# Kernel tuning notes

Hardware: AMD Instinct MI355X
Metric: run time of the kernel (lower is better)

The kernel has to match this reference:

```python
import jax, jax.numpy as jnp
import numpy as np

N_HEADS = 16


def setup_inputs() -> dict:
    key = jax.random.key(0)
    ks = jax.random.split(key, 7)
    B, S, D = 2, 2048, 1024
    x = jax.random.normal(ks[0], (B, S, D), dtype=jnp.float32)
    attn_mask = jax.random.normal(ks[1], (S, S), dtype=jnp.float32) * 0.1
    attn_bias = jax.random.normal(ks[2], (B, S, S), dtype=jnp.float32) * 0.1
    Wqkv = jax.random.normal(ks[3], (D, 3 * D), dtype=jnp.float32) * (D ** -0.5)
    bqkv = jnp.zeros((3 * D,), dtype=jnp.float32)
    Wout = jax.random.normal(ks[4], (D, D), dtype=jnp.float32) * (D ** -0.5)
    bout = jnp.zeros((D,), dtype=jnp.float32)
    return {"x": x, "attn_mask": attn_mask, "attn_bias": attn_bias,
            "Wqkv": Wqkv, "bqkv": bqkv, "Wout": Wout, "bout": bout}


def reference(x, attn_mask, attn_bias, Wqkv, bqkv, Wout, bout):
    B, S, D = x.shape
    H = N_HEADS
    hd = D // H
    # qkv projection: [B,S,3D] -> [3,B,H,S,hd]
    qkv = (x @ Wqkv + bqkv).reshape(B, S, 3, H, hd).transpose(2, 0, 3, 1, 4)
    q, k, v = qkv[0], qkv[1], qkv[2]
    scores = jnp.einsum('bhqd,bhkd->bhqk', q, k) / (hd ** 0.5)
    scores = scores + attn_mask[None, None, :, :] + attn_bias[:, None, :, :]
    attn = jax.nn.softmax(scores, axis=-1)  # dropout p=0.0 (eval)
    out = jnp.einsum('bhqk,bhkd->bhqd', attn, v)
    out = out.transpose(0, 2, 1, 3).reshape(B, S, D)
    return out @ Wout + bout
```

## Files before the change

kernel.cpp:

```cpp
#include <hip/hip_runtime.h>
#include <hip/hip_bf16.h>


#define S_LEN 2048
#define DMODEL 1024
#define NH 16
#define HD 64

typedef __bf16 bf16x8 __attribute__((ext_vector_type(8)));
typedef __bf16 bf16x4 __attribute__((ext_vector_type(4)));
typedef __bf16 bf16x2v __attribute__((ext_vector_type(2)));
typedef float f32x4 __attribute__((ext_vector_type(4)));

#define GLD_LDS16(g, l)                                              \
  __builtin_amdgcn_global_load_lds(                                  \
      (const __attribute__((address_space(1))) unsigned int*)(g),    \
      (__attribute__((address_space(3))) unsigned int*)(l), 16, 0, 0)

__global__ __launch_bounds__(256) void cvt_x(const float* __restrict__ X,
                                             __bf16* __restrict__ Xb) {
  int i = blockIdx.x * 256 + threadIdx.x;
  float4 v = ((const float4*)X)[i];
  bf16x4 o = {(__bf16)v.x, (__bf16)v.y, (__bf16)v.z, (__bf16)v.w};
  *(bf16x4*)&Xb[(size_t)i * 4] = o;
}

__global__ __launch_bounds__(256) void cvt_wt(const float* __restrict__ W,
                                              __bf16* __restrict__ Wt,
                                              int ncols) {
  __shared__ float tile[64][65];
  const int n0 = blockIdx.x * 64;
  const int k0 = blockIdx.y * 64;
  const int tid = threadIdx.x;
  {
    int c = tid & 63, r4 = tid >> 6;
#pragma unroll
    for (int p = 0; p < 16; ++p) {
      int r = r4 + p * 4;
      tile[r][c] = W[(size_t)(k0 + r) * ncols + n0 + c];
    }
  }
  __syncthreads();
  {
    int cc = (tid & 31) * 2, r8 = tid >> 5;
#pragma unroll
    for (int p = 0; p < 8; ++p) {
      int rr = r8 + p * 8;
      bf16x2v o = {(__bf16)tile[cc][rr], (__bf16)tile[cc + 1][rr]};
      *(bf16x2v*)&Wt[(size_t)(n0 + rr) * 1024 + k0 + cc] = o;
    }
  }
}

__global__ __launch_bounds__(256) void mb_fuse(const float* __restrict__ mask,
                                               const float* __restrict__ bias,
                                               __bf16* __restrict__ MB) {
  const int kt = blockIdx.x, qt = blockIdx.y, b = blockIdx.z;
  const int tid = threadIdx.x;
  const int r = tid >> 2;
  const int c0 = (tid & 3) * 16;
  const size_t qrow = (size_t)(qt * 64 + r);
  const float* mp = mask + qrow * S_LEN + kt * 64 + c0;
  const float* bp =
      bias + (size_t)b * S_LEN * S_LEN + qrow * S_LEN + kt * 64 + c0;
  __bf16* op = MB + (((size_t)(b * 32 + qt) * 32 + kt) * 4096) + r * 64 + c0;
#pragma unroll
  for (int e = 0; e < 4; ++e) {
    float4 m = *(const float4*)(mp + e * 4);
    float4 a = *(const float4*)(bp + e * 4);
    bf16x4 o = {(__bf16)(m.x + a.x), (__bf16)(m.y + a.y), (__bf16)(m.z + a.z),
                (__bf16)(m.w + a.w)};
    *(bf16x4*)(op + e * 4) = o;
  }
}

__global__ __launch_bounds__(256) void gemm_qkv_mfma(
    const __bf16* __restrict__ Xb, const __bf16* __restrict__ Wt,
    const float* __restrict__ bqkv, __bf16* __restrict__ Qb,
    __bf16* __restrict__ Kb, __bf16* __restrict__ Vtb) {
  __shared__ __align__(16) __bf16 As[128 * 32];
  __shared__ __align__(16) __bf16 Bs[128 * 32];
  const int tid = threadIdx.x;
  const int w = tid >> 6, lane = tid & 63;
  const int c = lane & 15, quad = lane >> 4;
  const int wm = w >> 1, wn = w & 1;
  const int rowBase = blockIdx.y * 128;
  const int colBase = blockIdx.x * 128;

  f32x4 acc[4][4] = {};

  const __bf16* gA0 =
      Xb + (size_t)(rowBase + w * 32 + (lane >> 2)) * 1024 + (lane & 3) * 8;
  const __bf16* gB0 =
      Wt + (size_t)(colBase + w * 32 + (lane >> 2)) * 1024 + (lane & 3) * 8;
  __bf16* lA0 = &As[(w * 32) * 32];
  __bf16* lB0 = &Bs[(w * 32) * 32];

  for (int k0 = 0; k0 < 1024; k0 += 32) {
    __syncthreads();
#pragma unroll
    for (int p = 0; p < 2; ++p) {
      GLD_LDS16(gA0 + (size_t)p * 16 * 1024 + k0, lA0 + p * 16 * 32);
      GLD_LDS16(gB0 + (size_t)p * 16 * 1024 + k0, lB0 + p * 16 * 32);
    }
    __syncthreads();

    bf16x8 af[4], bfr[4];
#pragma unroll
    for (int mt = 0; mt < 4; ++mt)
      af[mt] = *(const bf16x8*)&As[(wm * 64 + mt * 16 + c) * 32 + quad * 8];
#pragma unroll
    for (int nt = 0; nt < 4; ++nt)
      bfr[nt] = *(const bf16x8*)&Bs[(wn * 64 + nt * 16 + c) * 32 + quad * 8];
#pragma unroll
    for (int mt = 0; mt < 4; ++mt)
#pragma unroll
      for (int nt = 0; nt < 4; ++nt)
        acc[mt][nt] = __builtin_amdgcn_mfma_f32_16x16x32_bf16(
            af[mt], bfr[nt], acc[mt][nt], 0, 0, 0);
  }

#pragma unroll
  for (int mt = 0; mt < 4; ++mt) {
    int row0 = rowBase + wm * 64 + mt * 16 + quad * 4;
#pragma unroll
    for (int nt = 0; nt < 4; ++nt) {
      int col = colBase + wn * 64 + nt * 16 + c;
      float bias = bqkv[col];
      int three = col >> 10;
      int h = (col & 1023) >> 6;
      int d = col & 63;
#pragma unroll
      for (int r = 0; r < 4; ++r) {
        int rr = row0 + r;
        int bb = rr >> 11, s = rr & 2047;
        float val = acc[mt][nt][r] + bias;
        size_t ho = (size_t)(bb * NH + h);
        if (three == 0)
          Qb[(ho * S_LEN + s) * HD + d] = (__bf16)val;
        else if (three == 1)
          Kb[(ho * S_LEN + s) * HD + d] = (__bf16)val;
        else
          Vtb[(ho * HD + d) * S_LEN + s] = (__bf16)val;
      }
    }
  }
}

__global__ __launch_bounds__(256) void attn_mfma(
    const __bf16* __restrict__ Qb, const __bf16* __restrict__ Kb,
    const __bf16* __restrict__ Vtb, const __bf16* __restrict__ MB,
    __bf16* __restrict__ AOb) {
  const int qt = blockIdx.x, h = blockIdx.y, b = blockIdx.z;
  const int tid = threadIdx.x;
  const int w = tid >> 6;
  const int lane = tid & 63;
  const int c = lane & 15;
  const int quad = lane >> 4;

  __shared__ __align__(16) __bf16 Ks[64 * 72];
  __shared__ __align__(16) __bf16 Vs[64 * 72];
  __shared__ __align__(16) __bf16 Ps[64 * 72];
  __shared__ __align__(16) __bf16 MBs[64 * 64];

  const int qbase = qt * 64;
  const size_t headoff = (size_t)(b * NH + h) * S_LEN * HD;
  const __bf16* Qg = Qb + headoff + (size_t)qbase * HD;
  const __bf16* Kg = Kb + headoff;
  const __bf16* Vg = Vtb + headoff;
  const __bf16* MBg = MB + ((size_t)(b * 32 + qt) * 32) * 4096;

  bf16x8 qa0 = *(const bf16x8*)(Qg + (w * 16 + c) * HD + quad * 8);
  bf16x8 qa1 = *(const bf16x8*)(Qg + (w * 16 + c) * HD + quad * 8 + 32);

  f32x4 Oa[4] = {};
  float lsum[4] = {0.f, 0.f, 0.f, 0.f};

  for (int kt = 0; kt < 32; ++kt) {
    const int kbase = kt * 64;
    __syncthreads();
    {
      const __bf16* Kt = Kg + (size_t)kbase * HD;
      const __bf16* MBt = MBg + (size_t)kt * 4096;
#pragma unroll
      for (int p = 0; p < 2; ++p) {
        int ch = p * 256 + tid;
        int f = ch >> 3, c8 = (ch & 7) * 8;
        *(uint4*)&Ks[f * 72 + c8] = ((const uint4*)Kt)[ch];
        *(uint4*)&Vs[f * 72 + c8] =
            *(const uint4*)(Vg + (size_t)f * S_LEN + kbase + c8);
        GLD_LDS16(MBt + (size_t)ch * 8, &MBs[ch * 8]);
      }
    }
    __syncthreads();

    f32x4 sv[4];
#pragma unroll
    for (int ct = 0; ct < 4; ++ct) {
      f32x4 a = {};
      bf16x8 kf0 = *(const bf16x8*)&Ks[(ct * 16 + c) * 72 + quad * 8];
      bf16x8 kf1 = *(const bf16x8*)&Ks[(ct * 16 + c) * 72 + quad * 8 + 32];
      a = __builtin_amdgcn_mfma_f32_16x16x32_bf16(qa0, kf0, a, 0, 0, 0);
      a = __builtin_amdgcn_mfma_f32_16x16x32_bf16(qa1, kf1, a, 0, 0, 0);
      sv[ct] = a;
    }
#pragma unroll
    for (int ct = 0; ct < 4; ++ct)
#pragma unroll
      for (int r = 0; r < 4; ++r) {
        float mb = (float)MBs[(w * 16 + quad * 4 + r) * 64 + ct * 16 + c];
        float p = __expf(sv[ct][r] * 0.125f + mb - 8.0f);
        sv[ct][r] = p;
        lsum[r] += p;
        Ps[(w * 16 + quad * 4 + r) * 72 + ct * 16 + c] = (__bf16)p;
      }
    bf16x8 pf0 = *(const bf16x8*)&Ps[(w * 16 + c) * 72 + quad * 8];
    bf16x8 pf1 = *(const bf16x8*)&Ps[(w * 16 + c) * 72 + quad * 8 + 32];
#pragma unroll
    for (int ft = 0; ft < 4; ++ft) {
      bf16x8 vf0 = *(const bf16x8*)&Vs[(ft * 16 + c) * 72 + quad * 8];
      bf16x8 vf1 = *(const bf16x8*)&Vs[(ft * 16 + c) * 72 + quad * 8 + 32];
      Oa[ft] =
          __builtin_amdgcn_mfma_f32_16x16x32_bf16(pf0, vf0, Oa[ft], 0, 0, 0);
      Oa[ft] =
          __builtin_amdgcn_mfma_f32_16x16x32_bf16(pf1, vf1, Oa[ft], 0, 0, 0);
    }
  }
  float invl[4];
#pragma unroll
  for (int r = 0; r < 4; ++r) {
    float t = lsum[r];
    t += __shfl_xor(t, 1);
    t += __shfl_xor(t, 2);
    t += __shfl_xor(t, 4);
    t += __shfl_xor(t, 8);
    invl[r] = 1.0f / t;
  }
#pragma unroll
  for (int ft = 0; ft < 4; ++ft)
#pragma unroll
    for (int r = 0; r < 4; ++r)
      AOb[(size_t)(b * S_LEN + qbase + w * 16 + quad * 4 + r) * DMODEL +
          h * HD + ft * 16 + c] = (__bf16)(Oa[ft][r] * invl[r]);
}

__global__ __launch_bounds__(256) void gemm_out_mfma(
    const __bf16* __restrict__ AOb, const __bf16* __restrict__ Wt2,
    const float* __restrict__ bout, float* __restrict__ Out) {
  __shared__ __align__(16) __bf16 As[128 * 32];
  __shared__ __align__(16) __bf16 Bs[128 * 32];
  const int tid = threadIdx.x;
  const int w = tid >> 6, lane = tid & 63;
  const int c = lane & 15, quad = lane >> 4;
  const int wm = w >> 1, wn = w & 1;
  const int rowBase = blockIdx.y * 128;
  const int colBase = blockIdx.x * 128;

  f32x4 acc[4][4] = {};

  const __bf16* gA0 =
      AOb + (size_t)(rowBase + w * 32 + (lane >> 2)) * 1024 + (lane & 3) * 8;
  const __bf16* gB0 =
      Wt2 + (size_t)(colBase + w * 32 + (lane >> 2)) * 1024 + (lane & 3) * 8;
  __bf16* lA0 = &As[(w * 32) * 32];
  __bf16* lB0 = &Bs[(w * 32) * 32];

  for (int k0 = 0; k0 < 1024; k0 += 32) {
    __syncthreads();
#pragma unroll
    for (int p = 0; p < 2; ++p) {
      GLD_LDS16(gA0 + (size_t)p * 16 * 1024 + k0, lA0 + p * 16 * 32);
      GLD_LDS16(gB0 + (size_t)p * 16 * 1024 + k0, lB0 + p * 16 * 32);
    }
    __syncthreads();

    bf16x8 af[4], bfr[4];
#pragma unroll
    for (int mt = 0; mt < 4; ++mt)
      af[mt] = *(const bf16x8*)&As[(wm * 64 + mt * 16 + c) * 32 + quad * 8];
#pragma unroll
    for (int nt = 0; nt < 4; ++nt)
      bfr[nt] = *(const bf16x8*)&Bs[(wn * 64 + nt * 16 + c) * 32 + quad * 8];
#pragma unroll
    for (int mt = 0; mt < 4; ++mt)
#pragma unroll
      for (int nt = 0; nt < 4; ++nt)
        acc[mt][nt] = __builtin_amdgcn_mfma_f32_16x16x32_bf16(
            af[mt], bfr[nt], acc[mt][nt], 0, 0, 0);
  }

#pragma unroll
  for (int mt = 0; mt < 4; ++mt) {
    int row0 = rowBase + wm * 64 + mt * 16 + quad * 4;
#pragma unroll
    for (int nt = 0; nt < 4; ++nt) {
      int col = colBase + wn * 64 + nt * 16 + c;
      float bias = bout[col];
#pragma unroll
      for (int r = 0; r < 4; ++r)
        Out[(size_t)(row0 + r) * 1024 + col] = acc[mt][nt][r] + bias;
    }
  }
}

extern "C" void kernel_launch(void* const* d_in, const int* in_sizes, int n_in,
                              void* d_out, int out_size, void* d_ws,
                              size_t ws_size, hipStream_t stream) {
  const float* x = (const float*)d_in[0];
  const float* attn_mask = (const float*)d_in[1];
  const float* attn_bias = (const float*)d_in[2];
  const float* Wqkv = (const float*)d_in[3];
  const float* bqkv = (const float*)d_in[4];
  const float* Wout = (const float*)d_in[5];
  const float* bout = (const float*)d_in[6];
  float* out = (float*)d_out;

  __bf16* base = (__bf16*)d_ws;
  __bf16* Xb = base;
  __bf16* AOb = base;
  __bf16* Wt = base + 4194304;
  __bf16* Qb = base + 8388608;
  __bf16* Kb = base + 12582912;
  __bf16* Vtb = base + 16777216;
  __bf16* MB = base + 20971520;
  __bf16* Wt2 = base + 29360128;

  cvt_x<<<4096, 256, 0, stream>>>(x, Xb);
  cvt_wt<<<dim3(48, 16), 256, 0, stream>>>(Wqkv, Wt, 3072);
  cvt_wt<<<dim3(16, 16), 256, 0, stream>>>(Wout, Wt2, 1024);
  mb_fuse<<<dim3(32, 32, 2), 256, 0, stream>>>(attn_mask, attn_bias, MB);
  gemm_qkv_mfma<<<dim3(24, 32), 256, 0, stream>>>(Xb, Wt, bqkv, Qb, Kb, Vtb);
  attn_mfma<<<dim3(32, NH, 2), 256, 0, stream>>>(Qb, Kb, Vtb, MB, AOb);
  gemm_out_mfma<<<dim3(8, 32), 256, 0, stream>>>(AOb, Wt2, bout, out);
}
```

Baseline: 312.9 us.

## Prefetch next K/V/mask tile into registers while computing current tile

```diff
diff --git a/kernel.cpp b/kernel.cpp
--- a/kernel.cpp
+++ b/kernel.cpp
@@ -161,7 +161,7 @@
   __shared__ __align__(16) __bf16 Ks[64 * 72];
   __shared__ __align__(16) __bf16 Vs[64 * 72];
   __shared__ __align__(16) __bf16 Ps[64 * 72];
-  __shared__ __align__(16) __bf16 MBs[64 * 64];
+  __shared__ __align__(16) __bf16 MBs[64 * 72];
 
   const int qbase = qt * 64;
   const size_t headoff = (size_t)(b * NH + h) * S_LEN * HD;
@@ -173,26 +173,43 @@
   bf16x8 qa0 = *(const bf16x8*)(Qg + (w * 16 + c) * HD + quad * 8);
   bf16x8 qa1 = *(const bf16x8*)(Qg + (w * 16 + c) * HD + quad * 8 + 32);
 
+  int f0 = tid >> 3, c80 = (tid & 7) * 8;
+  int f1 = (256 + tid) >> 3, c81 = c80;
+
   f32x4 Oa[4] = {};
   float lsum[4] = {0.f, 0.f, 0.f, 0.f};
 
+  uint4 rK[2], rV[2], rMB[2];
+  {
+    const __bf16* Kt = Kg;
+    const __bf16* MBt = MBg;
+    rK[0] = *(const uint4*)(Kt + (size_t)f0 * HD + c80);
+    rK[1] = *(const uint4*)(Kt + (size_t)f1 * HD + c81);
+    rV[0] = *(const uint4*)(Vg + (size_t)f0 * S_LEN + c80);
+    rV[1] = *(const uint4*)(Vg + (size_t)f1 * S_LEN + c81);
+    rMB[0] = *(const uint4*)(MBt + (size_t)f0 * 64 + c80);
+    rMB[1] = *(const uint4*)(MBt + (size_t)f1 * 64 + c81);
+    *(uint4*)&Ks[f0 * 72 + c80] = rK[0];
+    *(uint4*)&Ks[f1 * 72 + c81] = rK[1];
+    *(uint4*)&Vs[f0 * 72 + c80] = rV[0];
+    *(uint4*)&Vs[f1 * 72 + c81] = rV[1];
+    *(uint4*)&MBs[f0 * 72 + c80] = rMB[0];
+    *(uint4*)&MBs[f1 * 72 + c81] = rMB[1];
+  }
+  __syncthreads();
+
   for (int kt = 0; kt < 32; ++kt) {
-    const int kbase = kt * 64;
-    __syncthreads();
-    {
-      const __bf16* Kt = Kg + (size_t)kbase * HD;
-      const __bf16* MBt = MBg + (size_t)kt * 4096;
-#pragma unroll
-      for (int p = 0; p < 2; ++p) {
-        int ch = p * 256 + tid;
-        int f = ch >> 3, c8 = (ch & 7) * 8;
-        *(uint4*)&Ks[f * 72 + c8] = ((const uint4*)Kt)[ch];
-        *(uint4*)&Vs[f * 72 + c8] =
-            *(const uint4*)(Vg + (size_t)f * S_LEN + kbase + c8);
-        GLD_LDS16(MBt + (size_t)ch * 8, &MBs[ch * 8]);
-      }
-    }
-    __syncthreads();
+    if (kt < 31) {
+      const int kb1 = (kt + 1) * 64;
+      const __bf16* Kt = Kg + (size_t)kb1 * HD;
+      const __bf16* MBt = MBg + (size_t)(kt + 1) * 4096;
+      rK[0] = *(const uint4*)(Kt + (size_t)f0 * HD + c80);
+      rK[1] = *(const uint4*)(Kt + (size_t)f1 * HD + c81);
+      rV[0] = *(const uint4*)(Vg + (size_t)f0 * S_LEN + kb1 + c80);
+      rV[1] = *(const uint4*)(Vg + (size_t)f1 * S_LEN + kb1 + c81);
+      rMB[0] = *(const uint4*)(MBt + (size_t)f0 * 64 + c80);
+      rMB[1] = *(const uint4*)(MBt + (size_t)f1 * 64 + c81);
+    }
 
     f32x4 sv[4];
 #pragma unroll
@@ -208,9 +225,8 @@
     for (int ct = 0; ct < 4; ++ct)
 #pragma unroll
       for (int r = 0; r < 4; ++r) {
-        float mb = (float)MBs[(w * 16 + quad * 4 + r) * 64 + ct * 16 + c];
+        float mb = (float)MBs[(w * 16 + quad * 4 + r) * 72 + ct * 16 + c];
         float p = __expf(sv[ct][r] * 0.125f + mb - 8.0f);
-        sv[ct][r] = p;
         lsum[r] += p;
         Ps[(w * 16 + quad * 4 + r) * 72 + ct * 16 + c] = (__bf16)p;
       }
@@ -224,6 +240,17 @@
           __builtin_amdgcn_mfma_f32_16x16x32_bf16(pf0, vf0, Oa[ft], 0, 0, 0);
       Oa[ft] =
           __builtin_amdgcn_mfma_f32_16x16x32_bf16(pf1, vf1, Oa[ft], 0, 0, 0);
+    }
+
+    if (kt < 31) {
+      __syncthreads();
+      *(uint4*)&Ks[f0 * 72 + c80] = rK[0];
+      *(uint4*)&Ks[f1 * 72 + c81] = rK[1];
+      *(uint4*)&Vs[f0 * 72 + c80] = rV[0];
+      *(uint4*)&Vs[f1 * 72 + c81] = rV[1];
+      *(uint4*)&MBs[f0 * 72 + c80] = rMB[0];
+      *(uint4*)&MBs[f1 * 72 + c81] = rMB[1];
+      __syncthreads();
     }
   }
   float invl[4];
```

Result: slower. 423.9 us (+35.5%).

## Double-buffer K/V via async LDS loads and prelayout mask-bias per lane

Applied to the files above, without the earlier changes.

```diff
diff --git a/kernel.cpp b/kernel.cpp
--- a/kernel.cpp
+++ b/kernel.cpp
@@ -57,21 +57,24 @@
                                                __bf16* __restrict__ MB) {
   const int kt = blockIdx.x, qt = blockIdx.y, b = blockIdx.z;
   const int tid = threadIdx.x;
-  const int r = tid >> 2;
-  const int c0 = (tid & 3) * 16;
-  const size_t qrow = (size_t)(qt * 64 + r);
-  const float* mp = mask + qrow * S_LEN + kt * 64 + c0;
+  const int w = tid >> 6, lane = tid & 63;
+  const int quad = lane >> 4, c = lane & 15;
+  const int row0 = qt * 64 + w * 16 + quad * 4;
+  const int col0 = kt * 64 + c;
+  const float* mp = mask + (size_t)row0 * S_LEN + col0;
   const float* bp =
-      bias + (size_t)b * S_LEN * S_LEN + qrow * S_LEN + kt * 64 + c0;
-  __bf16* op = MB + (((size_t)(b * 32 + qt) * 32 + kt) * 4096) + r * 64 + c0;
-#pragma unroll
-  for (int e = 0; e < 4; ++e) {
-    float4 m = *(const float4*)(mp + e * 4);
-    float4 a = *(const float4*)(bp + e * 4);
-    bf16x4 o = {(__bf16)(m.x + a.x), (__bf16)(m.y + a.y), (__bf16)(m.z + a.z),
-                (__bf16)(m.w + a.w)};
-    *(bf16x4*)(op + e * 4) = o;
-  }
+      bias + (size_t)b * S_LEN * S_LEN + (size_t)row0 * S_LEN + col0;
+  __bf16 vals[16];
+#pragma unroll
+  for (int ct = 0; ct < 4; ++ct)
+#pragma unroll
+    for (int r = 0; r < 4; ++r)
+      vals[ct * 4 + r] = (__bf16)(mp[(size_t)r * S_LEN + ct * 16] +
+                                  bp[(size_t)r * S_LEN + ct * 16]);
+  __bf16* op =
+      MB + (((size_t)(b * 32 + qt) * 32 + kt) * 4096) + (w * 64 + lane) * 16;
+  *(bf16x8*)op = *(bf16x8*)&vals[0];
+  *(bf16x8*)(op + 8) = *(bf16x8*)&vals[8];
 }
 
 __global__ __launch_bounds__(256) void gemm_qkv_mfma(
@@ -158,10 +161,9 @@
   const int c = lane & 15;
   const int quad = lane >> 4;
 
-  __shared__ __align__(16) __bf16 Ks[64 * 72];
-  __shared__ __align__(16) __bf16 Vs[64 * 72];
+  __shared__ __align__(16) __bf16 Ks[2][64 * 64];
+  __shared__ __align__(16) __bf16 Vs[2][64 * 64];
   __shared__ __align__(16) __bf16 Ps[64 * 72];
-  __shared__ __align__(16) __bf16 MBs[64 * 64];
 
   const int qbase = qt * 64;
   const size_t headoff = (size_t)(b * NH + h) * S_LEN * HD;
@@ -170,36 +172,47 @@
   const __bf16* Vg = Vtb + headoff;
   const __bf16* MBg = MB + ((size_t)(b * 32 + qt) * 32) * 4096;
 
+  const int f0 = tid >> 3, f1 = f0 + 32;
+  const int j = tid & 7;
+  const int sj0 = j ^ (f0 & 7);
+  const int sj1 = j ^ (f1 & 7);
+  const int lds0 = tid * 8;
+  const int lds1 = (256 + tid) * 8;
+
   bf16x8 qa0 = *(const bf16x8*)(Qg + (w * 16 + c) * HD + quad * 8);
   bf16x8 qa1 = *(const bf16x8*)(Qg + (w * 16 + c) * HD + quad * 8 + 32);
 
+  const int rs0 = (quad ^ (c & 7)) * 8;
+  const int rs1 = ((quad + 4) ^ (c & 7)) * 8;
+
   f32x4 Oa[4] = {};
   float lsum[4] = {0.f, 0.f, 0.f, 0.f};
 
+  GLD_LDS16(Kg + (size_t)f0 * HD + sj0 * 8, &Ks[0][lds0]);
+  GLD_LDS16(Kg + (size_t)f1 * HD + sj1 * 8, &Ks[0][lds1]);
+  GLD_LDS16(Vg + (size_t)f0 * S_LEN + sj0 * 8, &Vs[0][lds0]);
+  GLD_LDS16(Vg + (size_t)f1 * S_LEN + sj1 * 8, &Vs[0][lds1]);
+  __syncthreads();
+
   for (int kt = 0; kt < 32; ++kt) {
-    const int kbase = kt * 64;
-    __syncthreads();
-    {
-      const __bf16* Kt = Kg + (size_t)kbase * HD;
-      const __bf16* MBt = MBg + (size_t)kt * 4096;
-#pragma unroll
-      for (int p = 0; p < 2; ++p) {
-        int ch = p * 256 + tid;
-        int f = ch >> 3, c8 = (ch & 7) * 8;
-        *(uint4*)&Ks[f * 72 + c8] = ((const uint4*)Kt)[ch];
-        *(uint4*)&Vs[f * 72 + c8] =
-            *(const uint4*)(Vg + (size_t)f * S_LEN + kbase + c8);
-        GLD_LDS16(MBt + (size_t)ch * 8, &MBs[ch * 8]);
-      }
-    }
-    __syncthreads();
+    const int cur = kt & 1, nxt = cur ^ 1;
+    const __bf16* MBl = MBg + (size_t)kt * 4096 + (w * 64 + lane) * 16;
+    bf16x8 rMB0 = *(const bf16x8*)MBl;
+    bf16x8 rMB1 = *(const bf16x8*)(MBl + 8);
+    if (kt < 31) {
+      const int kb1 = (kt + 1) * 64;
+      GLD_LDS16(Kg + (size_t)(kb1 + f0) * HD + sj0 * 8, &Ks[nxt][lds0]);
+      GLD_LDS16(Kg + (size_t)(kb1 + f1) * HD + sj1 * 8, &Ks[nxt][lds1]);
+      GLD_LDS16(Vg + (size_t)f0 * S_LEN + kb1 + sj0 * 8, &Vs[nxt][lds0]);
+      GLD_LDS16(Vg + (size_t)f1 * S_LEN + kb1 + sj1 * 8, &Vs[nxt][lds1]);
+    }
 
     f32x4 sv[4];
 #pragma unroll
     for (int ct = 0; ct < 4; ++ct) {
       f32x4 a = {};
-      bf16x8 kf0 = *(const bf16x8*)&Ks[(ct * 16 + c) * 72 + quad * 8];
-      bf16x8 kf1 = *(const bf16x8*)&Ks[(ct * 16 + c) * 72 + quad * 8 + 32];
+      bf16x8 kf0 = *(const bf16x8*)&Ks[cur][(ct * 16 + c) * 64 + rs0];
+      bf16x8 kf1 = *(const bf16x8*)&Ks[cur][(ct * 16 + c) * 64 + rs1];
       a = __builtin_amdgcn_mfma_f32_16x16x32_bf16(qa0, kf0, a, 0, 0, 0);
       a = __builtin_amdgcn_mfma_f32_16x16x32_bf16(qa1, kf1, a, 0, 0, 0);
       sv[ct] = a;
@@ -208,9 +221,9 @@
     for (int ct = 0; ct < 4; ++ct)
 #pragma unroll
       for (int r = 0; r < 4; ++r) {
-        float mb = (float)MBs[(w * 16 + quad * 4 + r) * 64 + ct * 16 + c];
+        float mb = (ct < 2) ? (float)rMB0[ct * 4 + r]
+                            : (float)rMB1[(ct - 2) * 4 + r];
         float p = __expf(sv[ct][r] * 0.125f + mb - 8.0f);
-        sv[ct][r] = p;
         lsum[r] += p;
         Ps[(w * 16 + quad * 4 + r) * 72 + ct * 16 + c] = (__bf16)p;
       }
@@ -218,13 +231,15 @@
     bf16x8 pf1 = *(const bf16x8*)&Ps[(w * 16 + c) * 72 + quad * 8 + 32];
 #pragma unroll
     for (int ft = 0; ft < 4; ++ft) {
-      bf16x8 vf0 = *(const bf16x8*)&Vs[(ft * 16 + c) * 72 + quad * 8];
-      bf16x8 vf1 = *(const bf16x8*)&Vs[(ft * 16 + c) * 72 + quad * 8 + 32];
+      bf16x8 vf0 = *(const bf16x8*)&Vs[cur][(ft * 16 + c) * 64 + rs0];
+      bf16x8 vf1 = *(const bf16x8*)&Vs[cur][(ft * 16 + c) * 64 + rs1];
       Oa[ft] =
           __builtin_amdgcn_mfma_f32_16x16x32_bf16(pf0, vf0, Oa[ft], 0, 0, 0);
       Oa[ft] =
           __builtin_amdgcn_mfma_f32_16x16x32_bf16(pf1, vf1, Oa[ft], 0, 0, 0);
     }
+
+    __syncthreads();
   }
   float invl[4];
 #pragma unroll
```

After: 309.9 us. About the same (-0.9%).
